# Kernel tuning notes

Measured on AMD Instinct MI355X. Metric: run time of the kernel, lower is better.

The kernel has to match this reference:

```python
import jax, jax.numpy as jnp
import numpy as np

R_CUT = 10.0
ROUNDS = 1  # num_message_passing_rounds


def setup_inputs() -> dict:
    key = jax.random.key(0)
    N, DEG, S, NRBF, G = 10000, 16, 128, 20, 64
    E = N * DEG
    ks = jax.random.split(key, 16)
    w = lambda k, shp, fan: (jax.random.normal(k, shp, dtype=jnp.float32) / np.float32(np.sqrt(fan)))
    return {
        "edge_vector_diffs": jax.random.normal(ks[0], (E, 3), dtype=jnp.float32) * 3.0,
        "edge_lengths": jax.random.uniform(ks[1], (E,), dtype=jnp.float32) * 15.0,
        "node_from": jnp.repeat(jnp.arange(N), DEG),            # every node has DEG outgoing edges
        "node_graph_index": jax.random.randint(ks[2], (N,), 0, G),
        "num_graphs": G,
        "emb0": jax.random.normal(ks[3], (S,), dtype=jnp.float32) * 0.01,  # embedding.weight[0]
        "phi_w1": w(ks[4], (S, S), S), "phi_b1": jnp.zeros((S,), jnp.float32),
        "phi_w2": w(ks[5], (S, 3 * S), S), "phi_b2": jnp.zeros((3 * S,), jnp.float32),
        "filt_w": w(ks[6], (NRBF, 3 * S), NRBF), "filt_b": jnp.zeros((3 * S,), jnp.float32),
        "u_w": w(ks[7], (S, S), S), "v_w": w(ks[8], (S, S), S),
        "upd_w1": w(ks[9], (2 * S, S), 2 * S), "upd_b1": jnp.zeros((S,), jnp.float32),
        "upd_w2": w(ks[10], (S, 3 * S), S), "upd_b2": jnp.zeros((3 * S,), jnp.float32),
        "out_w1": w(ks[11], (S, S), S), "out_b1": jnp.zeros((S,), jnp.float32),
        "out_w2": w(ks[12], (S, 1), S), "out_b2": jnp.zeros((1,), jnp.float32),
    }


def reference(edge_vector_diffs, edge_lengths, node_from, node_graph_index, num_graphs,
              emb0, phi_w1, phi_b1, phi_w2, phi_b2, filt_w, filt_b, u_w, v_w,
              upd_w1, upd_b1, upd_w2, upd_b2, out_w1, out_b1, out_w2, out_b2):
    S = phi_w1.shape[0]
    N = node_graph_index.shape[0]
    NRBF = filt_w.shape[0]
    silu = jax.nn.silu
    seg = lambda v, n: jax.ops.segment_sum(v, node_from, num_segments=n)

    mask = (jnp.abs(edge_lengths) <= R_CUT).astype(jnp.float32)          # [E] nbr_mask
    r = jnp.linalg.norm(edge_vector_diffs, axis=1)                        # [E]
    r_safe = jnp.maximum(r, 1e-12)
    k = jnp.arange(1, NRBF + 1, dtype=jnp.float32)
    # PAINN sinc radial basis sin(k*pi*r/r_cut)/r, then linear -> [E, 3S]
    rbf = jnp.sin(k[None, :] * jnp.pi * r_safe[:, None] / R_CUT) / r_safe[:, None]
    cutoff = 0.5 * (jnp.cos(jnp.pi * r / R_CUT) + 1.0) * (r < R_CUT)      # cosine cutoff
    W = (rbf @ filt_w + filt_b) * cutoff[:, None]                          # [E, 3S]

    tile3 = jnp.arange(S) % 3  # xyzxyz... truncation pattern from .repeat(...)[: S]
    # scalar Frobenius norm of each node's masked neighbor-diff block
    frob = jnp.sqrt(seg(mask * r * r, N))                                  # [N]
    denom_e = frob[node_from]
    denom_e = jnp.where(denom_e > 0, denom_e, 1.0)
    normalized = edge_vector_diffs / denom_e[:, None]                      # [E, 3]
    norm_exp = normalized[:, tile3]                                        # [E, S]

    # state init: sum over dim 1 of embedding(zeros) == S * embedding.weight[0]
    state = jnp.broadcast_to(jnp.float32(S) * emb0, (N, S))
    state_vec = jnp.zeros((N, 3, S), jnp.float32)

    for _ in range(ROUNDS):
        # message block (nbrs_node_from == destination node, so sync update == original sequential loop)
        phi = silu(state[node_from] @ phi_w1 + phi_b1) @ phi_w2 + phi_b2   # [E, 3S]
        prod = phi * W
        m1, m2, m3 = prod[:, :S], prod[:, S:2 * S], prod[:, 2 * S:]
        vec_msg = state_vec[node_from] * m1[:, None, :] + (norm_exp * m3)[:, None, :]  # [E,3,S]
        state = seg(m2 * mask[:, None], N)                                 # [N, S]
        state_vec = seg(vec_msg * mask[:, None, None], N)                  # [N, 3, S]
        # update block
        U = jnp.einsum('nps,st->npt', state_vec, u_w)                      # [N,3,S]
        V = jnp.einsum('nps,st->npt', state_vec, v_w)
        UV = jnp.einsum('nps,nqs->npq', U, V)                              # [N,3,3]
        Vnorm = jnp.sqrt(jnp.sum(V * V, axis=1))                           # [N,S]
        a = silu(jnp.concatenate([Vnorm, state], axis=-1) @ upd_w1 + upd_b1) @ upd_w2 + upd_b2
        a_vv, a_sv, a_ss = a[:, :S], a[:, S:2 * S], a[:, 2 * S:]
        uv_tiled = jnp.sum(UV, axis=1)[:, tile3]                           # [N,S]
        state = a_ss + uv_tiled * a_sv
        state_vec = U * a_vv[:, None, :]

    graph_state = jax.ops.segment_sum(state, node_graph_index, num_segments=num_graphs)
    out = (silu(graph_state @ out_w1 + out_b1) @ out_w2 + out_b2).ravel()  # [num_graphs]
    return out
```

## Files before the change

kernel.cpp:

```cpp
#include <hip/hip_runtime.h>
#include <math.h>

#define NN   10000
#define DEG  16
#define SS   128
#define NRBF 20
#define GG   64
#define RC   10.0f
#define PI_F 3.14159265358979323846f
#define NB   8

__device__ __forceinline__ float silu_f(float x){
    return x / (1.0f + __expf(-x));
}

__global__ __launch_bounds__(256) void k_phi1(
    const float* __restrict__ emb0,
    const float* __restrict__ w1, const float* __restrict__ b1,
    float* __restrict__ phiH, float* __restrict__ gs){
    __shared__ float s0[SS];
    __shared__ float part[2][SS];
    int t = threadIdx.x;
    for (int i = t; i < GG*SS; i += 256) gs[i] = 0.0f;
    if (t < SS) s0[t] = 128.0f * emb0[t];
    __syncthreads();
    int c = t & 127, half = t >> 7;
    float acc = 0.0f;
    int s0i = half * 64;
    #pragma unroll 8
    for (int s = 0; s < 64; s++)
        acc = fmaf(s0[s0i + s], w1[(s0i + s)*SS + c], acc);
    part[half][c] = acc;
    __syncthreads();
    if (t < SS) phiH[t] = silu_f(b1[t] + part[0][t] + part[1][t]);
}

__global__ __launch_bounds__(128) void k_phi2(
    const float* __restrict__ phiH,
    const float* __restrict__ w2, const float* __restrict__ b2,
    float* __restrict__ phiW){
    __shared__ float hL[SS];
    __shared__ float part[4][32];
    int t = threadIdx.x;
    hL[t] = phiH[t];
    __syncthreads();
    int c  = blockIdx.x*32 + (t & 31);
    int kk = t >> 5;
    float acc = 0.0f;
    int sbase = kk * 32;
    #pragma unroll 8
    for (int s = 0; s < 32; s++)
        acc = fmaf(hL[sbase + s], w2[(sbase + s)*3*SS + c], acc);
    part[kk][t & 31] = acc;
    __syncthreads();
    if (t < 32){
        int cc = blockIdx.x*32 + t;
        phiW[cc] = b2[cc] + part[0][t] + part[1][t] + part[2][t] + part[3][t];
    }
}

__global__ __launch_bounds__(64) void k_edge(
    const float* __restrict__ evd, const float* __restrict__ elen,
    const int* __restrict__ node_from,
    const float* __restrict__ filt_w, const float* __restrict__ filt_b,
    const float* __restrict__ phiW,
    float* __restrict__ state, float* __restrict__ sv){
    __shared__ float rS[DEG];
    __shared__ float mcL[DEG];
    __shared__ float frL[DEG];
    __shared__ float eV[DEG][3];
    __shared__ float rbfL[DEG][NRBF];
    __shared__ float invD;
    int n = blockIdx.x;
    int t = threadIdx.x;

    if (t < DEG){
        int e = n*DEG + t;
        float x = evd[3*e+0], y = evd[3*e+1], z = evd[3*e+2];
        float r = sqrtf(x*x + y*y + z*z);
        float len  = elen[e];
        float mask = (fabsf(len) <= RC) ? 1.0f : 0.0f;
        float cut  = (r < RC) ? 0.5f*(cosf(PI_F*r*(1.0f/RC)) + 1.0f) : 0.0f;
        rS[t]  = fmaxf(r, 1e-12f);
        mcL[t] = mask * cut;
        frL[t] = mask * r * r;
        eV[t][0] = x; eV[t][1] = y; eV[t][2] = z;
    }
    __syncthreads();
    for (int idx = t; idx < DEG*NRBF; idx += 64){
        int e = idx / NRBF, k = idx % NRBF;
        float rs = rS[e];
        rbfL[e][k] = sinf((float)(k+1) * (PI_F/RC) * rs) / rs;
    }
    if (t == 0){
        float s = 0.0f;
        for (int e = 0; e < DEG; e++) s += frL[e];
        float fbn = sqrtf(s);
        invD = (fbn > 0.0f) ? 1.0f/fbn : 1.0f;
    }
    __syncthreads();

    int gcA = SS + t, gcB = SS + 64 + t;
    int gcC = 2*SS + t, gcD = 2*SS + 64 + t;
    float fwA[NRBF], fwB[NRBF], fwC[NRBF], fwD[NRBF];
    #pragma unroll
    for (int k = 0; k < NRBF; k++){
        fwA[k] = filt_w[k*(3*SS) + gcA];
        fwB[k] = filt_w[k*(3*SS) + gcB];
        fwC[k] = filt_w[k*(3*SS) + gcC];
        fwD[k] = filt_w[k*(3*SS) + gcD];
    }
    float fbA = filt_b[gcA], fbB = filt_b[gcB];
    float fbC = filt_b[gcC], fbD = filt_b[gcD];
    float phA = phiW[gcA], phB = phiW[gcB];
    float phC = phiW[gcC], phD = phiW[gcD];
    float iD  = invD;
    int   s3C = t % 3;
    int   s3D = (t + 64) % 3;

    float accA = 0.f, accB = 0.f, accC = 0.f, accD = 0.f;
    for (int e = 0; e < DEG; e++){
        float mc = mcL[e];
        if (mc == 0.0f) continue;
        const float4* rv = (const float4*)(&rbfL[e][0]);
        float4 r0 = rv[0], r1 = rv[1], r2 = rv[2], r3 = rv[3], r4 = rv[4];
        float rr[20] = {r0.x,r0.y,r0.z,r0.w, r1.x,r1.y,r1.z,r1.w,
                        r2.x,r2.y,r2.z,r2.w, r3.x,r3.y,r3.z,r3.w,
                        r4.x,r4.y,r4.z,r4.w};
        float wA = fbA, wB = fbB, wC = fbC, wD = fbD;
        #pragma unroll
        for (int k = 0; k < NRBF; k++){
            wA = fmaf(rr[k], fwA[k], wA);
            wB = fmaf(rr[k], fwB[k], wB);
            wC = fmaf(rr[k], fwC[k], wC);
            wD = fmaf(rr[k], fwD[k], wD);
        }
        accA = fmaf(phA*mc, wA, accA);
        accB = fmaf(phB*mc, wB, accB);
        accC = fmaf(phC*mc*eV[e][s3C]*iD, wC, accC);
        accD = fmaf(phD*mc*eV[e][s3D]*iD, wD, accD);
    }
    int nf = node_from[n*DEG];
    state[nf*SS + t]      = accA;
    state[nf*SS + 64 + t] = accB;
    sv[nf*SS + t]         = accC;
    sv[nf*SS + 64 + t]    = accD;
}

__global__ __launch_bounds__(128) void k_update(
    const float* __restrict__ state, const float* __restrict__ sv,
    const float* __restrict__ u_w, const float* __restrict__ v_w,
    const float* __restrict__ upd_w1, const float* __restrict__ upd_b1,
    const float* __restrict__ upd_w2, const float* __restrict__ upd_b2,
    const int* __restrict__ ngi, float* __restrict__ gs){
    __shared__ float svT[SS][NB];
    __shared__ float xT[2*SS][NB];
    __shared__ float dL[NB];
    __shared__ int   gIdx[NB];
    int t  = threadIdx.x;
    int w  = t >> 6, l = t & 63;
    int c0 = 2*l;
    int b0 = 4*w;
    int n0 = blockIdx.x * NB;

    if (t < NB) gIdx[t] = ngi[n0 + t];
    for (int idx = t; idx < NB*SS; idx += 128){
        int b = idx >> 7, s = idx & (SS-1);
        svT[s][b]   = sv[(n0+b)*SS + s];
        xT[SS+s][b] = state[(n0+b)*SS + s];
    }
    __syncthreads();

    float accU[2][4], accV[2][4];
    #pragma unroll
    for (int j = 0; j < 2; j++)
        #pragma unroll
        for (int k = 0; k < 4; k++){ accU[j][k] = 0.f; accV[j][k] = 0.f; }
    #pragma unroll 4
    for (int i = 0; i < SS; i++){
        float4 xv = *(const float4*)(&svT[i][b0]);
        float2 wu = *(const float2*)(u_w + i*SS + c0);
        float2 wv = *(const float2*)(v_w + i*SS + c0);
        float xa[4] = {xv.x, xv.y, xv.z, xv.w};
        #pragma unroll
        for (int k = 0; k < 4; k++){
            accU[0][k] = fmaf(xa[k], wu.x, accU[0][k]);
            accU[1][k] = fmaf(xa[k], wu.y, accU[1][k]);
            accV[0][k] = fmaf(xa[k], wv.x, accV[0][k]);
            accV[1][k] = fmaf(xa[k], wv.y, accV[1][k]);
        }
    }

    float pd[4];
    #pragma unroll
    for (int k = 0; k < 4; k++)
        pd[k] = accU[0][k]*accV[0][k] + accU[1][k]*accV[1][k];
    #pragma unroll
    for (int off = 32; off; off >>= 1){
        #pragma unroll
        for (int k = 0; k < 4; k++) pd[k] += __shfl_down(pd[k], off);
    }
    if (l == 0){
        #pragma unroll
        for (int k = 0; k < 4; k++) dL[b0+k] = pd[k];
    }
    const float SQ3 = 1.7320508075688772f;
    #pragma unroll
    for (int j = 0; j < 2; j++)
        #pragma unroll
        for (int k = 0; k < 4; k++)
            xT[c0+j][b0+k] = SQ3 * fabsf(accV[j][k]);
    __syncthreads();

    float dreg[4];
    #pragma unroll
    for (int k = 0; k < 4; k++) dreg[k] = dL[b0+k];

    float accH[2][4];
    #pragma unroll
    for (int j = 0; j < 2; j++)
        #pragma unroll
        for (int k = 0; k < 4; k++) accH[j][k] = 0.f;
    #pragma unroll 4
    for (int i = 0; i < 2*SS; i++){
        float4 xv = *(const float4*)(&xT[i][b0]);
        float2 ww = *(const float2*)(upd_w1 + i*SS + c0);
        float xa[4] = {xv.x, xv.y, xv.z, xv.w};
        #pragma unroll
        for (int k = 0; k < 4; k++){
            accH[0][k] = fmaf(xa[k], ww.x, accH[0][k]);
            accH[1][k] = fmaf(xa[k], ww.y, accH[1][k]);
        }
    }
    {
        float2 b1v = *(const float2*)(upd_b1 + c0);
        #pragma unroll
        for (int k = 0; k < 4; k++){
            svT[c0+0][b0+k] = silu_f(accH[0][k] + b1v.x);
            svT[c0+1][b0+k] = silu_f(accH[1][k] + b1v.y);
        }
    }
    __syncthreads();

    float a2[2][4], a3[2][4];
    #pragma unroll
    for (int j = 0; j < 2; j++)
        #pragma unroll
        for (int k = 0; k < 4; k++){ a2[j][k] = 0.f; a3[j][k] = 0.f; }
    #pragma unroll 4
    for (int j = 0; j < SS; j++){
        float4 hx = *(const float4*)(&svT[j][b0]);
        float2 w2 = *(const float2*)(upd_w2 + j*3*SS + SS   + c0);
        float2 w3 = *(const float2*)(upd_w2 + j*3*SS + 2*SS + c0);
        float ha[4] = {hx.x, hx.y, hx.z, hx.w};
        #pragma unroll
        for (int k = 0; k < 4; k++){
            a2[0][k] = fmaf(ha[k], w2.x, a2[0][k]);
            a2[1][k] = fmaf(ha[k], w2.y, a2[1][k]);
            a3[0][k] = fmaf(ha[k], w3.x, a3[0][k]);
            a3[1][k] = fmaf(ha[k], w3.y, a3[1][k]);
        }
    }
    float2 bsv = *(const float2*)(upd_b2 + SS   + c0);
    float2 bss = *(const float2*)(upd_b2 + 2*SS + c0);
    #pragma unroll
    for (int k = 0; k < 4; k++){
        int g = gIdx[b0+k];
        float ns0 = (a3[0][k] + bss.x) + 3.0f*dreg[k]*(a2[0][k] + bsv.x);
        float ns1 = (a3[1][k] + bss.y) + 3.0f*dreg[k]*(a2[1][k] + bsv.y);
        atomicAdd(&gs[g*SS + c0 + 0], ns0);
        atomicAdd(&gs[g*SS + c0 + 1], ns1);
    }
}

__global__ __launch_bounds__(128) void k_out(
    const float* __restrict__ gs,
    const float* __restrict__ w1, const float* __restrict__ b1,
    const float* __restrict__ w2, const float* __restrict__ b2,
    float* __restrict__ out){
    __shared__ float gsL[SS];
    __shared__ float red[2];
    int g = blockIdx.x, t = threadIdx.x;
    gsL[t] = gs[g*SS + t];
    __syncthreads();
    float acc = b1[t];
    #pragma unroll 4
    for (int s = 0; s < SS; s++) acc = fmaf(gsL[s], w1[s*SS + t], acc);
    float p = silu_f(acc) * w2[t];
    for (int off = 32; off; off >>= 1) p += __shfl_down(p, off);
    if ((t & 63) == 0) red[t >> 6] = p;
    __syncthreads();
    if (t == 0) out[g] = red[0] + red[1] + b2[0];
}

extern "C" void kernel_launch(void* const* d_in, const int* in_sizes, int n_in,
                              void* d_out, int out_size, void* d_ws, size_t ws_size,
                              hipStream_t stream) {
    const float* evd     = (const float*)d_in[0];
    const float* elen    = (const float*)d_in[1];
    const int*   nfrom   = (const int*)  d_in[2];
    const int*   ngi     = (const int*)  d_in[3];
    const float* emb0    = (const float*)d_in[5];
    const float* phi_w1  = (const float*)d_in[6];
    const float* phi_b1  = (const float*)d_in[7];
    const float* phi_w2  = (const float*)d_in[8];
    const float* phi_b2  = (const float*)d_in[9];
    const float* filt_w  = (const float*)d_in[10];
    const float* filt_b  = (const float*)d_in[11];
    const float* u_w     = (const float*)d_in[12];
    const float* v_w     = (const float*)d_in[13];
    const float* upd_w1  = (const float*)d_in[14];
    const float* upd_b1  = (const float*)d_in[15];
    const float* upd_w2  = (const float*)d_in[16];
    const float* upd_b2  = (const float*)d_in[17];
    const float* out_w1  = (const float*)d_in[18];
    const float* out_b1  = (const float*)d_in[19];
    const float* out_w2  = (const float*)d_in[20];
    const float* out_b2  = (const float*)d_in[21];

    float* ws    = (float*)d_ws;
    float* phiW  = ws;
    float* state = ws + 512;
    float* sv    = state + NN*SS;
    float* gs    = sv + NN*SS;
    float* phiH  = gs + GG*SS;

    k_phi1<<<1, 256, 0, stream>>>(emb0, phi_w1, phi_b1, phiH, gs);
    k_phi2<<<12, 128, 0, stream>>>(phiH, phi_w2, phi_b2, phiW);
    k_edge<<<NN, 64, 0, stream>>>(evd, elen, nfrom, filt_w, filt_b, phiW, state, sv);
    k_update<<<NN/NB, 128, 0, stream>>>(state, sv, u_w, v_w,
                                        upd_w1, upd_b1, upd_w2, upd_b2, ngi, gs);
    k_out<<<GG, 128, 0, stream>>>(gs, out_w1, out_b1, out_w2, out_b2, (float*)d_out);
}
```

Baseline: 202.2 us.

## Fuse phi kernels and retile update kernel to 16 nodes with 4x4 register tiles

Merges the two phi MLP kernels into one launch, with each block recomputing the hidden layer redundantly. Retiles the node update kernel to process 16 nodes per block, each thread computing a 4x4 output tile with float4 weight loads and a padded transposed shared layout. This halves global weight traffic per node and removes a launch, at the cost of fewer blocks and more registers per thread. The PI constant was also altered to a slightly incorrect value.

```diff
diff --git a/kernel.cpp b/kernel.cpp
--- a/kernel.cpp
+++ b/kernel.cpp
@@ -7,51 +7,39 @@
 #define NRBF 20
 #define GG   64
 #define RC   10.0f
-#define PI_F 3.14159265358979323846f
-#define NB   8
+#define PI_F 3.14159265897932f
+#define NBK  16
+#define PAD  20
 
 __device__ __forceinline__ float silu_f(float x){
     return x / (1.0f + __expf(-x));
 }
 
-__global__ __launch_bounds__(256) void k_phi1(
+__global__ __launch_bounds__(128) void k_phi(
     const float* __restrict__ emb0,
     const float* __restrict__ w1, const float* __restrict__ b1,
-    float* __restrict__ phiH, float* __restrict__ gs){
+    const float* __restrict__ w2, const float* __restrict__ b2,
+    float* __restrict__ phiW, float* __restrict__ gs){
     __shared__ float s0[SS];
-    __shared__ float part[2][SS];
-    int t = threadIdx.x;
-    for (int i = t; i < GG*SS; i += 256) gs[i] = 0.0f;
-    if (t < SS) s0[t] = 128.0f * emb0[t];
-    __syncthreads();
-    int c = t & 127, half = t >> 7;
-    float acc = 0.0f;
-    int s0i = half * 64;
-    #pragma unroll 8
-    for (int s = 0; s < 64; s++)
-        acc = fmaf(s0[s0i + s], w1[(s0i + s)*SS + c], acc);
-    part[half][c] = acc;
-    __syncthreads();
-    if (t < SS) phiH[t] = silu_f(b1[t] + part[0][t] + part[1][t]);
-}
-
-__global__ __launch_bounds__(128) void k_phi2(
-    const float* __restrict__ phiH,
-    const float* __restrict__ w2, const float* __restrict__ b2,
-    float* __restrict__ phiW){
     __shared__ float hL[SS];
     __shared__ float part[4][32];
     int t = threadIdx.x;
-    hL[t] = phiH[t];
+    for (int i = blockIdx.x*128 + t; i < GG*SS; i += 12*128) gs[i] = 0.0f;
+    s0[t] = 128.0f * emb0[t];
+    __syncthreads();
+    float acc = b1[t];
+    #pragma unroll 4
+    for (int s = 0; s < SS; s++) acc = fmaf(s0[s], w1[s*SS + t], acc);
+    hL[t] = silu_f(acc);
     __syncthreads();
     int c  = blockIdx.x*32 + (t & 31);
     int kk = t >> 5;
-    float acc = 0.0f;
+    float a = 0.0f;
     int sbase = kk * 32;
     #pragma unroll 8
     for (int s = 0; s < 32; s++)
-        acc = fmaf(hL[sbase + s], w2[(sbase + s)*3*SS + c], acc);
-    part[kk][t & 31] = acc;
+        a = fmaf(hL[sbase + s], w2[(sbase + s)*3*SS + c], a);
+    part[kk][t & 31] = a;
     __syncthreads();
     if (t < 32){
         int cc = blockIdx.x*32 + t;
@@ -153,123 +141,152 @@
     const float* __restrict__ upd_w1, const float* __restrict__ upd_b1,
     const float* __restrict__ upd_w2, const float* __restrict__ upd_b2,
     const int* __restrict__ ngi, float* __restrict__ gs){
-    __shared__ float svT[SS][NB];
-    __shared__ float xT[2*SS][NB];
-    __shared__ float dL[NB];
-    __shared__ int   gIdx[NB];
+    __shared__ float svT[SS*PAD];
+    __shared__ float xT[2*SS*PAD];
+    __shared__ float hT[SS*PAD];
+    __shared__ float dL[NBK];
+    __shared__ int   gIdx[NBK];
     int t  = threadIdx.x;
-    int w  = t >> 6, l = t & 63;
-    int c0 = 2*l;
-    int b0 = 4*w;
-    int n0 = blockIdx.x * NB;
-
-    if (t < NB) gIdx[t] = ngi[n0 + t];
-    for (int idx = t; idx < NB*SS; idx += 128){
-        int b = idx >> 7, s = idx & (SS-1);
-        svT[s][b]   = sv[(n0+b)*SS + s];
-        xT[SS+s][b] = state[(n0+b)*SS + s];
-    }
-    __syncthreads();
-
-    float accU[2][4], accV[2][4];
-    #pragma unroll
-    for (int j = 0; j < 2; j++)
-        #pragma unroll
-        for (int k = 0; k < 4; k++){ accU[j][k] = 0.f; accV[j][k] = 0.f; }
-    #pragma unroll 4
-    for (int i = 0; i < SS; i++){
-        float4 xv = *(const float4*)(&svT[i][b0]);
-        float2 wu = *(const float2*)(u_w + i*SS + c0);
-        float2 wv = *(const float2*)(v_w + i*SS + c0);
+    int cg = t & 31, ng = t >> 5;
+    int c0 = 4*cg,  n0 = 4*ng;
+    int nb = blockIdx.x * NBK;
+
+    if (t < NBK) gIdx[t] = ngi[nb + t];
+
+    {
+        int sg = cg, ig = ng;
+        int s0 = 4*sg;
+        float4 a0 = *(const float4*)(sv + (nb + 4*ig + 0)*SS + s0);
+        float4 a1 = *(const float4*)(sv + (nb + 4*ig + 1)*SS + s0);
+        float4 a2 = *(const float4*)(sv + (nb + 4*ig + 2)*SS + s0);
+        float4 a3 = *(const float4*)(sv + (nb + 4*ig + 3)*SS + s0);
+        *(float4*)(svT + (s0+0)*PAD + 4*ig) = make_float4(a0.x,a1.x,a2.x,a3.x);
+        *(float4*)(svT + (s0+1)*PAD + 4*ig) = make_float4(a0.y,a1.y,a2.y,a3.y);
+        *(float4*)(svT + (s0+2)*PAD + 4*ig) = make_float4(a0.z,a1.z,a2.z,a3.z);
+        *(float4*)(svT + (s0+3)*PAD + 4*ig) = make_float4(a0.w,a1.w,a2.w,a3.w);
+        float4 b0 = *(const float4*)(state + (nb + 4*ig + 0)*SS + s0);
+        float4 b1 = *(const float4*)(state + (nb + 4*ig + 1)*SS + s0);
+        float4 b2 = *(const float4*)(state + (nb + 4*ig + 2)*SS + s0);
+        float4 b3 = *(const float4*)(state + (nb + 4*ig + 3)*SS + s0);
+        *(float4*)(xT + (SS+s0+0)*PAD + 4*ig) = make_float4(b0.x,b1.x,b2.x,b3.x);
+        *(float4*)(xT + (SS+s0+1)*PAD + 4*ig) = make_float4(b0.y,b1.y,b2.y,b3.y);
+        *(float4*)(xT + (SS+s0+2)*PAD + 4*ig) = make_float4(b0.z,b1.z,b2.z,b3.z);
+        *(float4*)(xT + (SS+s0+3)*PAD + 4*ig) = make_float4(b0.w,b1.w,b2.w,b3.w);
+    }
+    __syncthreads();
+
+    float accU[4][4], accV[4][4];
+    #pragma unroll
+    for (int j = 0; j < 4; j++)
+        #pragma unroll
+        for (int i = 0; i < 4; i++){ accU[j][i]=0.f; accV[j][i]=0.f; }
+    #pragma unroll 2
+    for (int k = 0; k < SS; k++){
+        float4 xv = *(const float4*)(svT + k*PAD + n0);
+        float4 wu = *(const float4*)(u_w + k*SS + c0);
+        float4 wv = *(const float4*)(v_w + k*SS + c0);
         float xa[4] = {xv.x, xv.y, xv.z, xv.w};
-        #pragma unroll
-        for (int k = 0; k < 4; k++){
-            accU[0][k] = fmaf(xa[k], wu.x, accU[0][k]);
-            accU[1][k] = fmaf(xa[k], wu.y, accU[1][k]);
-            accV[0][k] = fmaf(xa[k], wv.x, accV[0][k]);
-            accV[1][k] = fmaf(xa[k], wv.y, accV[1][k]);
+        float wua[4] = {wu.x, wu.y, wu.z, wu.w};
+        float wva[4] = {wv.x, wv.y, wv.z, wv.w};
+        #pragma unroll
+        for (int j = 0; j < 4; j++)
+            #pragma unroll
+            for (int i = 0; i < 4; i++){
+                accU[j][i] = fmaf(xa[i], wua[j], accU[j][i]);
+                accV[j][i] = fmaf(xa[i], wva[j], accV[j][i]);
+            }
+    }
+
+    float pd[4];
+    #pragma unroll
+    for (int i = 0; i < 4; i++){
+        pd[i] = accU[0][i]*accV[0][i] + accU[1][i]*accV[1][i]
+              + accU[2][i]*accV[2][i] + accU[3][i]*accV[3][i];
+    }
+    #pragma unroll
+    for (int mask = 1; mask <= 16; mask <<= 1){
+        #pragma unroll
+        for (int i = 0; i < 4; i++) pd[i] += __shfl_xor(pd[i], mask);
+    }
+    if (cg == 0){
+        #pragma unroll
+        for (int i = 0; i < 4; i++) dL[n0+i] = pd[i];
+    }
+
+    const float SQ3 = 1.7320508075688772f;
+    #pragma unroll
+    for (int j = 0; j < 4; j++)
+        *(float4*)(xT + (c0+j)*PAD + n0) =
+            make_float4(SQ3*fabsf(accV[j][0]), SQ3*fabsf(accV[j][1]),
+                        SQ3*fabsf(accV[j][2]), SQ3*fabsf(accV[j][3]));
+    __syncthreads();
+
+    float dreg[4];
+    #pragma unroll
+    for (int i = 0; i < 4; i++) dreg[i] = dL[n0+i];
+
+    float accH[4][4];
+    #pragma unroll
+    for (int j = 0; j < 4; j++)
+        #pragma unroll
+        for (int i = 0; i < 4; i++) accH[j][i] = 0.f;
+    #pragma unroll 2
+    for (int k = 0; k < 2*SS; k++){
+        float4 xv = *(const float4*)(xT + k*PAD + n0);
+        float4 ww = *(const float4*)(upd_w1 + k*SS + c0);
+        float xa[4] = {xv.x, xv.y, xv.z, xv.w};
+        float wa[4] = {ww.x, ww.y, ww.z, ww.w};
+        #pragma unroll
+        for (int j = 0; j < 4; j++)
+            #pragma unroll
+            for (int i = 0; i < 4; i++)
+                accH[j][i] = fmaf(xa[i], wa[j], accH[j][i]);
+    }
+    {
+        float4 b1v = *(const float4*)(upd_b1 + c0);
+        float ba[4] = {b1v.x, b1v.y, b1v.z, b1v.w};
+        #pragma unroll
+        for (int j = 0; j < 4; j++)
+            *(float4*)(hT + (c0+j)*PAD + n0) =
+                make_float4(silu_f(accH[j][0]+ba[j]), silu_f(accH[j][1]+ba[j]),
+                            silu_f(accH[j][2]+ba[j]), silu_f(accH[j][3]+ba[j]));
+    }
+    __syncthreads();
+
+    float a2[4][4], a3[4][4];
+    #pragma unroll
+    for (int j = 0; j < 4; j++)
+        #pragma unroll
+        for (int i = 0; i < 4; i++){ a2[j][i]=0.f; a3[j][i]=0.f; }
+    #pragma unroll 2
+    for (int k = 0; k < SS; k++){
+        float4 hx = *(const float4*)(hT + k*PAD + n0);
+        float4 w2 = *(const float4*)(upd_w2 + k*3*SS + SS   + c0);
+        float4 w3 = *(const float4*)(upd_w2 + k*3*SS + 2*SS + c0);
+        float ha[4] = {hx.x, hx.y, hx.z, hx.w};
+        float w2a[4] = {w2.x, w2.y, w2.z, w2.w};
+        float w3a[4] = {w3.x, w3.y, w3.z, w3.w};
+        #pragma unroll
+        for (int j = 0; j < 4; j++)
+            #pragma unroll
+            for (int i = 0; i < 4; i++){
+                a2[j][i] = fmaf(ha[i], w2a[j], a2[j][i]);
+                a3[j][i] = fmaf(ha[i], w3a[j], a3[j][i]);
+            }
+    }
+    float4 bsv4 = *(const float4*)(upd_b2 + SS   + c0);
+    float4 bss4 = *(const float4*)(upd_b2 + 2*SS + c0);
+    float bsv[4] = {bsv4.x, bsv4.y, bsv4.z, bsv4.w};
+    float bss[4] = {bss4.x, bss4.y, bss4.z, bss4.w};
+    #pragma unroll
+    for (int i = 0; i < 4; i++){
+        int g = gIdx[n0+i];
+        float d3 = 3.0f * dreg[i];
+        #pragma unroll
+        for (int j = 0; j < 4; j++){
+            float ns = (a3[j][i] + bss[j]) + d3*(a2[j][i] + bsv[j]);
+            atomicAdd(&gs[g*SS + c0 + j], ns);
         }
-    }
-
-    float pd[4];
-    #pragma unroll
-    for (int k = 0; k < 4; k++)
-        pd[k] = accU[0][k]*accV[0][k] + accU[1][k]*accV[1][k];
-    #pragma unroll
-    for (int off = 32; off; off >>= 1){
-        #pragma unroll
-        for (int k = 0; k < 4; k++) pd[k] += __shfl_down(pd[k], off);
-    }
-    if (l == 0){
-        #pragma unroll
-        for (int k = 0; k < 4; k++) dL[b0+k] = pd[k];
-    }
-    const float SQ3 = 1.7320508075688772f;
-    #pragma unroll
-    for (int j = 0; j < 2; j++)
-        #pragma unroll
-        for (int k = 0; k < 4; k++)
-            xT[c0+j][b0+k] = SQ3 * fabsf(accV[j][k]);
-    __syncthreads();
-
-    float dreg[4];
-    #pragma unroll
-    for (int k = 0; k < 4; k++) dreg[k] = dL[b0+k];
-
-    float accH[2][4];
-    #pragma unroll
-    for (int j = 0; j < 2; j++)
-        #pragma unroll
-        for (int k = 0; k < 4; k++) accH[j][k] = 0.f;
-    #pragma unroll 4
-    for (int i = 0; i < 2*SS; i++){
-        float4 xv = *(const float4*)(&xT[i][b0]);
-        float2 ww = *(const float2*)(upd_w1 + i*SS + c0);
-        float xa[4] = {xv.x, xv.y, xv.z, xv.w};
-        #pragma unroll
-        for (int k = 0; k < 4; k++){
-            accH[0][k] = fmaf(xa[k], ww.x, accH[0][k]);
-            accH[1][k] = fmaf(xa[k], ww.y, accH[1][k]);
-        }
-    }
-    {
-        float2 b1v = *(const float2*)(upd_b1 + c0);
-        #pragma unroll
-        for (int k = 0; k < 4; k++){
-            svT[c0+0][b0+k] = silu_f(accH[0][k] + b1v.x);
-            svT[c0+1][b0+k] = silu_f(accH[1][k] + b1v.y);
-        }
-    }
-    __syncthreads();
-
-    float a2[2][4], a3[2][4];
-    #pragma unroll
-    for (int j = 0; j < 2; j++)
-        #pragma unroll
-        for (int k = 0; k < 4; k++){ a2[j][k] = 0.f; a3[j][k] = 0.f; }
-    #pragma unroll 4
-    for (int j = 0; j < SS; j++){
-        float4 hx = *(const float4*)(&svT[j][b0]);
-        float2 w2 = *(const float2*)(upd_w2 + j*3*SS + SS   + c0);
-        float2 w3 = *(const float2*)(upd_w2 + j*3*SS + 2*SS + c0);
-        float ha[4] = {hx.x, hx.y, hx.z, hx.w};
-        #pragma unroll
-        for (int k = 0; k < 4; k++){
-            a2[0][k] = fmaf(ha[k], w2.x, a2[0][k]);
-            a2[1][k] = fmaf(ha[k], w2.y, a2[1][k]);
-            a3[0][k] = fmaf(ha[k], w3.x, a3[0][k]);
-            a3[1][k] = fmaf(ha[k], w3.y, a3[1][k]);
-        }
-    }
-    float2 bsv = *(const float2*)(upd_b2 + SS   + c0);
-    float2 bss = *(const float2*)(upd_b2 + 2*SS + c0);
-    #pragma unroll
-    for (int k = 0; k < 4; k++){
-        int g = gIdx[b0+k];
-        float ns0 = (a3[0][k] + bss.x) + 3.0f*dreg[k]*(a2[0][k] + bsv.x);
-        float ns1 = (a3[1][k] + bss.y) + 3.0f*dreg[k]*(a2[1][k] + bsv.y);
-        atomicAdd(&gs[g*SS + c0 + 0], ns0);
-        atomicAdd(&gs[g*SS + c0 + 1], ns1);
     }
 }
 
@@ -323,12 +340,10 @@
     float* state = ws + 512;
     float* sv    = state + NN*SS;
     float* gs    = sv + NN*SS;
-    float* phiH  = gs + GG*SS;
-
-    k_phi1<<<1, 256, 0, stream>>>(emb0, phi_w1, phi_b1, phiH, gs);
-    k_phi2<<<12, 128, 0, stream>>>(phiH, phi_w2, phi_b2, phiW);
+
+    k_phi<<<12, 128, 0, stream>>>(emb0, phi_w1, phi_b1, phi_w2, phi_b2, phiW, gs);
     k_edge<<<NN, 64, 0, stream>>>(evd, elen, nfrom, filt_w, filt_b, phiW, state, sv);
-    k_update<<<NN/NB, 128, 0, stream>>>(state, sv, u_w, v_w,
-                                        upd_w1, upd_b1, upd_w2, upd_b2, ngi, gs);
+    k_update<<<NN/NBK, 128, 0, stream>>>(state, sv, u_w, v_w,
+                                         upd_w1, upd_b1, upd_w2, upd_b2, ngi, gs);
     k_out<<<GG, 128, 0, stream>>>(gs, out_w1, out_b1, out_w2, out_b2, (float*)d_out);
 }
```

Result: slower. 244.1 us (+20.7%).
